# Kernel optimization log

Measured on AMD Instinct MI355X. Metric: run time of the kernel, lower is better.

## Reference

```python
import jax, jax.numpy as jnp
import numpy as np

S = 1024      # seq_len (capped by module's precomputed rows/cols tables)
B = 8         # batch
E = 512       # embed_dim
PD = 192      # pos_dim
H = 8         # num_heads
QHD = 32      # query_head_dim (== key_head_dim)
PHD = 4       # pos_head_dim
IN_DIM = (2 * QHD + PHD) * H  # 544


def setup_inputs() -> dict:
    key = jax.random.key(0)
    k0, k1, k2, k3 = jax.random.split(key, 4)
    x = jax.random.normal(k0, (S, B, E), jnp.float32)
    pos_emb = jax.random.normal(k1, (B, 2 * S - 1, PD), jnp.float32)
    # ScaledLinear(embed_dim, in_proj_dim, initial_scale=query_head_dim**-0.25)
    W_in = jax.random.normal(k2, (E, IN_DIM), jnp.float32) * (QHD ** -0.25) / np.sqrt(E).astype(np.float32)
    b_in = jnp.zeros((IN_DIM,), jnp.float32)
    # ScaledLinear(pos_dim, num_heads*pos_head_dim, bias=False, initial_scale=0.05)
    W_pos = jax.random.normal(k3, (PD, H * PHD), jnp.float32) * (0.05 / np.sqrt(PD).astype(np.float32))
    return {"x": x, "pos_emb": pos_emb, "W_in": W_in, "b_in": b_in, "W_pos": W_pos}


def reference(x, pos_emb, W_in, b_in, W_pos):
    s, b, _ = x.shape
    h, qhd, phd = H, QHD, PHD
    qdim = h * qhd

    proj = x @ W_in + b_in                      # [S, B, 544]
    q = proj[..., :qdim].reshape(s, b, h, qhd)          # [S,B,H,Dq]
    k = proj[..., qdim:2 * qdim].reshape(s, b, h, qhd)  # [S,B,H,Dq]
    p = proj[..., 2 * qdim:].reshape(s, b, h, phd)      # [S,B,H,Dp]

    # attn_scores[h,b,i,j] = q_i . k_j
    attn_scores = jnp.einsum('sbhd,tbhd->hbst', q, k)   # [H,B,S,S]

    # positional projection: [B, 2S-1, H, Dp]
    pe = (pos_emb @ W_pos).reshape(b, 2 * s - 1, h, phd)
    pos_scores = jnp.einsum('sbhd,bnhd->hbsn', p, pe)   # [H,B,S,2S-1]

    # relative skew: index[i,j] = (S-1-i) + j  (matches rows[-S:]+cols gather)
    idx = (s - 1) - jnp.arange(s)[:, None] + jnp.arange(s)[None, :]  # [S,S]
    idx_b = jnp.broadcast_to(idx[None, None], (h, b, s, s))
    rel = jnp.take_along_axis(pos_scores, idx_b, axis=-1)            # [H,B,S,S]

    return jax.nn.softmax(attn_scores + rel, axis=-1)
```

## Files before the change

### kernel.cpp

```cpp
#include <hip/hip_runtime.h>
#include <hip/hip_fp16.h>

#define S_LEN 1024
#define BATCH 8
#define EMB 512
#define POSD 192
#define NH 8
#define QHD 32
#define PHD 4
#define IN_DIM 544
#define QDIM 256
#define NPOS 2047

typedef _Float16 half8 __attribute__((ext_vector_type(8)));
typedef _Float16 half4_t __attribute__((ext_vector_type(4)));
typedef _Float16 half2_t __attribute__((ext_vector_type(2)));
typedef float f32x4 __attribute__((ext_vector_type(4)));

static __device__ __forceinline__ float fdot2(half2_t a, half2_t b, float c) {
#if __has_builtin(__builtin_amdgcn_fdot2)
  return __builtin_amdgcn_fdot2(a, b, c, false);
#else
  return c + (float)a[0] * (float)b[0] + (float)a[1] * (float)b[1];
#endif
}

__global__ __launch_bounds__(256) void wconv_kernel(const float* __restrict__ W_in,
                                                    const float* __restrict__ W_pos,
                                                    _Float16* __restrict__ Wt,
                                                    _Float16* __restrict__ WtP) {
  const int blk = blockIdx.x;
  const int tid = threadIdx.x;
  if (blk < 72) {
    __shared__ float T[64][65];
    const int bx = blk % 9;
    const int by = blk / 9;
    const int n0 = bx * 64, e0 = by * 64;
    const int r = tid >> 4, c4 = (tid & 15) * 4;
    if (n0 + c4 < IN_DIM) {
      #pragma unroll
      for (int rr = 0; rr < 64; rr += 16) {
        f32x4 v = *(const f32x4*)(W_in + (size_t)(e0 + r + rr) * IN_DIM + n0 + c4);
        T[r + rr][c4] = v[0]; T[r + rr][c4 + 1] = v[1];
        T[r + rr][c4 + 2] = v[2]; T[r + rr][c4 + 3] = v[3];
      }
    }
    __syncthreads();
    const int nl = tid >> 2, ec = (tid & 3) * 16;
    const int n = n0 + nl;
    if (n < IN_DIM) {
      half8 h0, h1;
      #pragma unroll
      for (int j = 0; j < 8; ++j) {
        h0[j] = (_Float16)T[ec + j][nl];
        h1[j] = (_Float16)T[ec + 8 + j][nl];
      }
      *(half8*)(Wt + (size_t)n * EMB + e0 + ec) = h0;
      *(half8*)(Wt + (size_t)n * EMB + e0 + ec + 8) = h1;
    }
  } else {
    for (int i = tid; i < 32 * POSD; i += 256) {
      int c = i / POSD, k = i % POSD;
      WtP[i] = (_Float16)W_pos[(size_t)k * 32 + c];
    }
  }
}

__global__ __launch_bounds__(256) void pe_kernel(const float* __restrict__ pos_emb,
                                                 const _Float16* __restrict__ WtP,
                                                 _Float16* __restrict__ pe16) {
  __shared__ __align__(16) _Float16 As[64][200];
  const int b = blockIdx.y, chunk = blockIdx.x;
  const int n0 = chunk * 64;
  const int tid = threadIdx.x;
  const int row = tid >> 2, sc = tid & 3;
  const bool rowok = (n0 + row) < NPOS;
  const float* src = pos_emb + ((size_t)b * NPOS + n0 + row) * POSD + sc * 48;
  #pragma unroll
  for (int j = 0; j < 6; ++j) {
    f32x4 v0 = {}, v1 = {};
    if (rowok) { v0 = *(const f32x4*)(src + j * 8); v1 = *(const f32x4*)(src + j * 8 + 4); }
    half8 h;
    #pragma unroll
    for (int t = 0; t < 4; ++t) { h[t] = (_Float16)v0[t]; h[4 + t] = (_Float16)v1[t]; }
    *(half8*)&As[row][sc * 48 + j * 8] = h;
  }
  __syncthreads();
  const int w = tid >> 6, l = tid & 63, g = l >> 4, lg = l & 15;
  f32x4 acc0 = {}, acc1 = {};
  #pragma unroll
  for (int kk = 0; kk < POSD; kk += 32) {
    half8 aF = *(const half8*)&As[w * 16 + lg][kk + g * 8];
    half8 b0 = *(const half8*)(WtP + (size_t)lg * POSD + kk + g * 8);
    half8 b1 = *(const half8*)(WtP + (size_t)(16 + lg) * POSD + kk + g * 8);
    acc0 = __builtin_amdgcn_mfma_f32_16x16x32_f16(aF, b0, acc0, 0, 0, 0);
    acc1 = __builtin_amdgcn_mfma_f32_16x16x32_f16(aF, b1, acc1, 0, 0, 0);
  }
  f32x4 accs[2] = {acc0, acc1};
  #pragma unroll
  for (int t = 0; t < 2; ++t) {
    int c = t * 16 + lg, h = c >> 2, d = c & 3;
    _Float16* dst = pe16 + ((size_t)(b * NH + h) * NPOS) * PHD + d;
    #pragma unroll
    for (int r = 0; r < 4; ++r) {
      int n = n0 + w * 16 + 4 * g + r;
      if (n < NPOS) dst[(size_t)n * PHD] = (_Float16)accs[t][r];
    }
  }
}

__global__ __launch_bounds__(256) void proj_kernel(const float* __restrict__ x,
                                                   const _Float16* __restrict__ Wt,
                                                   const float* __restrict__ bias,
                                                   _Float16* __restrict__ q16,
                                                   _Float16* __restrict__ k16,
                                                   _Float16* __restrict__ p16) {
  __shared__ __align__(16) _Float16 As[64][40];
  __shared__ __align__(16) _Float16 Bs[64][40];
  const int m0 = blockIdx.x * 64;
  const int n0 = blockIdx.y * 64;
  const int tid = threadIdx.x;
  const int w = tid >> 6, l = tid & 63, g = l >> 4, lg = l & 15;
  const int wm = w >> 1, wn = w & 1;
  const int srow = tid >> 2, sc = tid & 3;

  f32x4 acc[2][2] = {};

  for (int k0 = 0; k0 < EMB; k0 += 32) {
    const float* asrc = x + (size_t)(m0 + srow) * EMB + k0 + sc * 8;
    f32x4 a0 = *(const f32x4*)asrc;
    f32x4 a1 = *(const f32x4*)(asrc + 4);
    half8 ah;
    #pragma unroll
    for (int j = 0; j < 4; ++j) { ah[j] = (_Float16)a0[j]; ah[4 + j] = (_Float16)a1[j]; }
    int nrow = n0 + srow;
    half8 bh8 = {};
    if (nrow < IN_DIM) bh8 = *(const half8*)(Wt + (size_t)nrow * EMB + k0 + sc * 8);
    *(half8*)&As[srow][sc * 8] = ah;
    *(half8*)&Bs[srow][sc * 8] = bh8;
    __syncthreads();
    half8 aF0 = *(const half8*)&As[wm * 32 + lg][g * 8];
    half8 aF1 = *(const half8*)&As[wm * 32 + 16 + lg][g * 8];
    half8 bF0 = *(const half8*)&Bs[wn * 32 + lg][g * 8];
    half8 bF1 = *(const half8*)&Bs[wn * 32 + 16 + lg][g * 8];
    acc[0][0] = __builtin_amdgcn_mfma_f32_16x16x32_f16(aF0, bF0, acc[0][0], 0, 0, 0);
    acc[0][1] = __builtin_amdgcn_mfma_f32_16x16x32_f16(aF0, bF1, acc[0][1], 0, 0, 0);
    acc[1][0] = __builtin_amdgcn_mfma_f32_16x16x32_f16(aF1, bF0, acc[1][0], 0, 0, 0);
    acc[1][1] = __builtin_amdgcn_mfma_f32_16x16x32_f16(aF1, bF1, acc[1][1], 0, 0, 0);
    __syncthreads();
  }

  #pragma unroll
  for (int sm = 0; sm < 2; ++sm)
    #pragma unroll
    for (int sn = 0; sn < 2; ++sn)
      #pragma unroll
      for (int r = 0; r < 4; ++r) {
        int m = m0 + wm * 32 + sm * 16 + 4 * g + r;
        int n = n0 + wn * 32 + sn * 16 + lg;
        if (n < IN_DIM) {
          float v = acc[sm][sn][r] + bias[n];
          _Float16 hv = (_Float16)v;
          int s = m >> 3, b = m & 7;
          if (n < QDIM) {
            int h = n >> 5, d = n & 31;
            q16[(((size_t)(b * NH + h)) * S_LEN + s) * QHD + d] = hv;
          } else if (n < 2 * QDIM) {
            int n2 = n - QDIM;
            int h = n2 >> 5, d = n2 & 31;
            k16[(((size_t)(b * NH + h)) * S_LEN + s) * QHD + d] = hv;
          } else {
            int n2 = n - 2 * QDIM;
            int h = n2 >> 2, d = n2 & 3;
            p16[(((size_t)(b * NH + h)) * S_LEN + s) * PHD + d] = hv;
          }
        }
      }
}

__global__ __launch_bounds__(256, 4) void attn_kernel(const _Float16* __restrict__ q16,
                                                      const _Float16* __restrict__ k16,
                                                      const _Float16* __restrict__ p16,
                                                      const _Float16* __restrict__ pe16,
                                                      float* __restrict__ out) {
  __shared__ __align__(16) _Float16 peLDS[1040 * 4];
  __shared__ float wred[4][16];
  __shared__ __align__(16) float sbuf[4][16][68];
  const int bid = blockIdx.x;
  const int swz = (bid & 7) * 512 + (bid >> 3);
  const int bh = swz >> 6;
  const int rblk = swz & 63;
  const int b = bh >> 3, h = bh & 7;
  const int i0 = rblk * 16;
  const int tid = threadIdx.x;
  const int w = tid >> 6, l = tid & 63, g = l >> 4, lg = l & 15;
  const int nlo = S_LEN - 16 - i0;

  for (int it = tid; it < 1039; it += 256) {
    *(uint2*)&peLDS[it * 4] =
        *(const uint2*)&pe16[((size_t)bh * NPOS + nlo + it) * 4];
  }

  const _Float16* qbase = q16 + ((size_t)bh * S_LEN + i0) * QHD;
  half8 qF = *(const half8*)(qbase + lg * QHD + g * 8);

  const _Float16* pbase = p16 + ((size_t)bh * S_LEN + i0 + lg) * PHD;
  half2_t pq0 = *(const half2_t*)(pbase);
  half2_t pq1 = *(const half2_t*)(pbase + 2);

  __syncthreads();

  const _Float16* kbase = k16 + (size_t)bh * S_LEN * QHD;
  const int jw = w * 256;
  f32x4 zero = {};
  float s = 0.f;
  half4_t probs[16];

  #pragma unroll
  for (int ct = 0; ct < 16; ++ct) {
    int j = jw + ct * 16 + lg;
    half8 kF = *(const half8*)(kbase + (size_t)j * QHD + g * 8);
    f32x4 a = __builtin_amdgcn_mfma_f32_16x16x32_f16(kF, qF, zero, 0, 0, 0);
    int nl0 = 15 - lg + jw + ct * 16 + 4 * g;
    half4_t ph;
    #pragma unroll
    for (int r = 0; r < 4; ++r) {
      half4_t pv4 = *(const half4_t*)&peLDS[(nl0 + r) * 4];
      half2_t lo = {pv4[0], pv4[1]};
      half2_t hi = {pv4[2], pv4[3]};
      float sc = fdot2(pq1, hi, fdot2(pq0, lo, a[r]));
      float e = __expf(sc - 6.0f);
      s += e;
      ph[r] = (_Float16)e;
    }
    probs[ct] = ph;
  }

  s += __shfl_xor(s, 16);
  s += __shfl_xor(s, 32);
  if (g == 0) wred[w][lg] = s;
  __syncthreads();
  s = (wred[0][lg] + wred[1][lg]) + (wred[2][lg] + wred[3][lg]);
  const float inv = 1.0f / s;

  const size_t orow0 = ((size_t)(h * BATCH + b) * S_LEN + i0) * S_LEN;
  #pragma unroll
  for (int chunk = 0; chunk < 4; ++chunk) {
    #pragma unroll
    for (int cc = 0; cc < 4; ++cc) {
      half4_t ph = probs[chunk * 4 + cc];
      f32x4 v;
      #pragma unroll
      for (int r = 0; r < 4; ++r) v[r] = (float)ph[r] * inv;
      *(f32x4*)&sbuf[w][lg][cc * 16 + 4 * g] = v;
    }
    asm volatile("s_waitcnt lgkmcnt(0)" ::: "memory");
    __builtin_amdgcn_sched_barrier(0);
    #pragma unroll
    for (int k2 = 0; k2 < 4; ++k2) {
      int rr = k2 * 4 + g;
      f32x4 v = *(const f32x4*)&sbuf[w][rr][lg * 4];
      __builtin_nontemporal_store(
          v, (f32x4*)(out + orow0 + (size_t)rr * S_LEN + jw + chunk * 64 + lg * 4));
    }
    asm volatile("s_waitcnt lgkmcnt(0)" ::: "memory");
    __builtin_amdgcn_sched_barrier(0);
  }
}

extern "C" void kernel_launch(void* const* d_in, const int* in_sizes, int n_in,
                              void* d_out, int out_size, void* d_ws, size_t ws_size,
                              hipStream_t stream) {
  const float* x = (const float*)d_in[0];
  const float* pos_emb = (const float*)d_in[1];
  const float* W_in = (const float*)d_in[2];
  const float* b_in = (const float*)d_in[3];
  const float* W_pos = (const float*)d_in[4];
  float* out = (float*)d_out;

  char* ws = (char*)d_ws;
  _Float16* Wt = (_Float16*)(ws);
  _Float16* q16 = (_Float16*)(ws + 557056);
  _Float16* k16 = (_Float16*)(ws + 557056 + 4194304);
  _Float16* p16 = (_Float16*)(ws + 557056 + 2 * 4194304);
  _Float16* pe16 = (_Float16*)(ws + 557056 + 2 * 4194304 + 524288);
  _Float16* WtP = p16;

  wconv_kernel<<<dim3(73), dim3(256), 0, stream>>>(W_in, W_pos, Wt, WtP);
  pe_kernel<<<dim3(32, BATCH), dim3(256), 0, stream>>>(pos_emb, WtP, pe16);
  proj_kernel<<<dim3(128, 9), dim3(256), 0, stream>>>(x, Wt, b_in, q16, k16, p16);
  attn_kernel<<<dim3(4096), dim3(256), 0, stream>>>(q16, k16, p16, pe16, out);
}
```

Before: 88.15 us.

## Restructure projection GEMM to stage full x rows once and stream weights

The projection kernel now loads a 32-row slab of x across the whole K dimension into LDS once, converting it to fp16, and covers all 544 output columns in a single block. Each of 8 waves owns 4-5 column tiles and reads weight fragments directly from global memory. This removes the per-K-step double __syncthreads and the 9x re-reading of x across column blocks. In exchange, weights are read without LDS staging, per-block LDS grows, and register use rises with 10 accumulators per wave.

```diff
diff --git a/kernel.cpp b/kernel.cpp
--- a/kernel.cpp
+++ b/kernel.cpp
@@ -109,57 +109,60 @@
   }
 }
 
-__global__ __launch_bounds__(256) void proj_kernel(const float* __restrict__ x,
+__global__ __launch_bounds__(512) void proj_kernel(const float* __restrict__ x,
                                                    const _Float16* __restrict__ Wt,
                                                    const float* __restrict__ bias,
                                                    _Float16* __restrict__ q16,
                                                    _Float16* __restrict__ k16,
                                                    _Float16* __restrict__ p16) {
-  __shared__ __align__(16) _Float16 As[64][40];
-  __shared__ __align__(16) _Float16 Bs[64][40];
-  const int m0 = blockIdx.x * 64;
-  const int n0 = blockIdx.y * 64;
-  const int tid = threadIdx.x;
+  __shared__ __align__(16) _Float16 As[32][520];
+  const int m0 = blockIdx.x * 32;
+  const int tid = threadIdx.x;
+  {
+    const int row = tid >> 4, c0 = (tid & 15) * 32;
+    const float* src = x + (size_t)(m0 + row) * EMB + c0;
+    #pragma unroll
+    for (int jj = 0; jj < 4; ++jj) {
+      f32x4 v0 = *(const f32x4*)(src + jj * 8);
+      f32x4 v1 = *(const f32x4*)(src + jj * 8 + 4);
+      half8 h;
+      #pragma unroll
+      for (int t = 0; t < 4; ++t) { h[t] = (_Float16)v0[t]; h[4 + t] = (_Float16)v1[t]; }
+      *(half8*)&As[row][c0 + jj * 8] = h;
+    }
+  }
+  __syncthreads();
+
   const int w = tid >> 6, l = tid & 63, g = l >> 4, lg = l & 15;
-  const int wm = w >> 1, wn = w & 1;
-  const int srow = tid >> 2, sc = tid & 3;
-
-  f32x4 acc[2][2] = {};
-
-  for (int k0 = 0; k0 < EMB; k0 += 32) {
-    const float* asrc = x + (size_t)(m0 + srow) * EMB + k0 + sc * 8;
-    f32x4 a0 = *(const f32x4*)asrc;
-    f32x4 a1 = *(const f32x4*)(asrc + 4);
-    half8 ah;
-    #pragma unroll
-    for (int j = 0; j < 4; ++j) { ah[j] = (_Float16)a0[j]; ah[4 + j] = (_Float16)a1[j]; }
-    int nrow = n0 + srow;
-    half8 bh8 = {};
-    if (nrow < IN_DIM) bh8 = *(const half8*)(Wt + (size_t)nrow * EMB + k0 + sc * 8);
-    *(half8*)&As[srow][sc * 8] = ah;
-    *(half8*)&Bs[srow][sc * 8] = bh8;
-    __syncthreads();
-    half8 aF0 = *(const half8*)&As[wm * 32 + lg][g * 8];
-    half8 aF1 = *(const half8*)&As[wm * 32 + 16 + lg][g * 8];
-    half8 bF0 = *(const half8*)&Bs[wn * 32 + lg][g * 8];
-    half8 bF1 = *(const half8*)&Bs[wn * 32 + 16 + lg][g * 8];
-    acc[0][0] = __builtin_amdgcn_mfma_f32_16x16x32_f16(aF0, bF0, acc[0][0], 0, 0, 0);
-    acc[0][1] = __builtin_amdgcn_mfma_f32_16x16x32_f16(aF0, bF1, acc[0][1], 0, 0, 0);
-    acc[1][0] = __builtin_amdgcn_mfma_f32_16x16x32_f16(aF1, bF0, acc[1][0], 0, 0, 0);
-    acc[1][1] = __builtin_amdgcn_mfma_f32_16x16x32_f16(aF1, bF1, acc[1][1], 0, 0, 0);
-    __syncthreads();
-  }
-
-  #pragma unroll
-  for (int sm = 0; sm < 2; ++sm)
-    #pragma unroll
-    for (int sn = 0; sn < 2; ++sn)
-      #pragma unroll
-      for (int r = 0; r < 4; ++r) {
-        int m = m0 + wm * 32 + sm * 16 + 4 * g + r;
-        int n = n0 + wn * 32 + sn * 16 + lg;
-        if (n < IN_DIM) {
-          float v = acc[sm][sn][r] + bias[n];
+  const int NT = (w < 2) ? 5 : 4;
+  f32x4 acc[2][5] = {};
+
+  for (int kk = 0; kk < EMB; kk += 32) {
+    half8 a0 = *(const half8*)&As[lg][kk + g * 8];
+    half8 a1 = *(const half8*)&As[16 + lg][kk + g * 8];
+    #pragma unroll
+    for (int tt = 0; tt < 5; ++tt) {
+      if (tt < NT) {
+        int t = w + 8 * tt;
+        half8 bF = *(const half8*)(Wt + (size_t)(t * 16 + lg) * EMB + kk + g * 8);
+        acc[0][tt] = __builtin_amdgcn_mfma_f32_16x16x32_f16(a0, bF, acc[0][tt], 0, 0, 0);
+        acc[1][tt] = __builtin_amdgcn_mfma_f32_16x16x32_f16(a1, bF, acc[1][tt], 0, 0, 0);
+      }
+    }
+  }
+
+  #pragma unroll
+  for (int tt = 0; tt < 5; ++tt) {
+    if (tt < NT) {
+      int t = w + 8 * tt;
+      int n = t * 16 + lg;
+      float bv = bias[n];
+      #pragma unroll
+      for (int fm = 0; fm < 2; ++fm) {
+        #pragma unroll
+        for (int r = 0; r < 4; ++r) {
+          int m = m0 + fm * 16 + 4 * g + r;
+          float v = acc[fm][tt][r] + bv;
           _Float16 hv = (_Float16)v;
           int s = m >> 3, b = m & 7;
           if (n < QDIM) {
@@ -176,6 +179,8 @@
           }
         }
       }
+    }
+  }
 }
 
 __global__ __launch_bounds__(256, 4) void attn_kernel(const _Float16* __restrict__ q16,
@@ -288,6 +293,6 @@
 
   wconv_kernel<<<dim3(73), dim3(256), 0, stream>>>(W_in, W_pos, Wt, WtP);
   pe_kernel<<<dim3(32, BATCH), dim3(256), 0, stream>>>(pos_emb, WtP, pe16);
-  proj_kernel<<<dim3(128, 9), dim3(256), 0, stream>>>(x, Wt, b_in, q16, k16, p16);
+  proj_kernel<<<dim3(256), dim3(512), 0, stream>>>(x, Wt, b_in, q16, k16, p16);
   attn_kernel<<<dim3(4096), dim3(256), 0, stream>>>(q16, k16, p16, pe16, out);
 }
```

New measurement: 94.43 us. 1.07x slower.

## Merge weight conversion and positional projection into one prep kernel; XCD-aware proj tiling

Applied to the files above, without the earlier changes.

Fuses the W_in transpose/convert kernel and the positional-embedding projection kernel into a single launch. Each pe block now converts W_pos into LDS itself instead of reading a global fp16 copy, which removes one launch and the dependency between the two. The proj kernel grid is flattened to 1D and remapped so that consecutive blocks on the same XCD share M tiles, aiming for better L2 reuse of x. The cost is redundant W_pos conversion in every pe block and higher LDS use per block.

```diff
diff --git a/kernel.cpp b/kernel.cpp
--- a/kernel.cpp
+++ b/kernel.cpp
@@ -25,14 +25,16 @@
 #endif
 }
 
-__global__ __launch_bounds__(256) void wconv_kernel(const float* __restrict__ W_in,
-                                                    const float* __restrict__ W_pos,
-                                                    _Float16* __restrict__ Wt,
-                                                    _Float16* __restrict__ WtP) {
+__global__ __launch_bounds__(256) void prep_kernel(const float* __restrict__ W_in,
+                                                   const float* __restrict__ W_pos,
+                                                   const float* __restrict__ pos_emb,
+                                                   _Float16* __restrict__ Wt,
+                                                   _Float16* __restrict__ pe16) {
+  __shared__ __align__(16) char smem[38400];
   const int blk = blockIdx.x;
   const int tid = threadIdx.x;
   if (blk < 72) {
-    __shared__ float T[64][65];
+    float (*T)[65] = reinterpret_cast<float(*)[65]>(smem);
     const int bx = blk % 9;
     const int by = blk / 9;
     const int n0 = bx * 64, e0 = by * 64;
@@ -59,52 +61,52 @@
       *(half8*)(Wt + (size_t)n * EMB + e0 + ec + 8) = h1;
     }
   } else {
-    for (int i = tid; i < 32 * POSD; i += 256) {
-      int c = i / POSD, k = i % POSD;
-      WtP[i] = (_Float16)W_pos[(size_t)k * 32 + c];
-    }
-  }
-}
-
-__global__ __launch_bounds__(256) void pe_kernel(const float* __restrict__ pos_emb,
-                                                 const _Float16* __restrict__ WtP,
-                                                 _Float16* __restrict__ pe16) {
-  __shared__ __align__(16) _Float16 As[64][200];
-  const int b = blockIdx.y, chunk = blockIdx.x;
-  const int n0 = chunk * 64;
-  const int tid = threadIdx.x;
-  const int row = tid >> 2, sc = tid & 3;
-  const bool rowok = (n0 + row) < NPOS;
-  const float* src = pos_emb + ((size_t)b * NPOS + n0 + row) * POSD + sc * 48;
-  #pragma unroll
-  for (int j = 0; j < 6; ++j) {
-    f32x4 v0 = {}, v1 = {};
-    if (rowok) { v0 = *(const f32x4*)(src + j * 8); v1 = *(const f32x4*)(src + j * 8 + 4); }
-    half8 h;
-    #pragma unroll
-    for (int t = 0; t < 4; ++t) { h[t] = (_Float16)v0[t]; h[4 + t] = (_Float16)v1[t]; }
-    *(half8*)&As[row][sc * 48 + j * 8] = h;
-  }
-  __syncthreads();
-  const int w = tid >> 6, l = tid & 63, g = l >> 4, lg = l & 15;
-  f32x4 acc0 = {}, acc1 = {};
-  #pragma unroll
-  for (int kk = 0; kk < POSD; kk += 32) {
-    half8 aF = *(const half8*)&As[w * 16 + lg][kk + g * 8];
-    half8 b0 = *(const half8*)(WtP + (size_t)lg * POSD + kk + g * 8);
-    half8 b1 = *(const half8*)(WtP + (size_t)(16 + lg) * POSD + kk + g * 8);
-    acc0 = __builtin_amdgcn_mfma_f32_16x16x32_f16(aF, b0, acc0, 0, 0, 0);
-    acc1 = __builtin_amdgcn_mfma_f32_16x16x32_f16(aF, b1, acc1, 0, 0, 0);
-  }
-  f32x4 accs[2] = {acc0, acc1};
-  #pragma unroll
-  for (int t = 0; t < 2; ++t) {
-    int c = t * 16 + lg, h = c >> 2, d = c & 3;
-    _Float16* dst = pe16 + ((size_t)(b * NH + h) * NPOS) * PHD + d;
-    #pragma unroll
-    for (int r = 0; r < 4; ++r) {
-      int n = n0 + w * 16 + 4 * g + r;
-      if (n < NPOS) dst[(size_t)n * PHD] = (_Float16)accs[t][r];
+    _Float16 (*As)[200] = reinterpret_cast<_Float16(*)[200]>(smem);
+    _Float16 (*Wl)[200] = reinterpret_cast<_Float16(*)[200]>(smem + 25600);
+    const int id = blk - 72;
+    const int chunk = id & 31, b = id >> 5;
+    const int n0 = chunk * 64;
+    #pragma unroll
+    for (int p = 0; p < 6; ++p) {
+      int f = (p * 256 + tid) * 4;
+      f32x4 v = *(const f32x4*)(W_pos + f);
+      int k = f >> 5, c = f & 31;
+      #pragma unroll
+      for (int t = 0; t < 4; ++t) Wl[c + t][k] = (_Float16)v[t];
+    }
+    const int row = tid >> 2, sc = tid & 3;
+    const bool rowok = (n0 + row) < NPOS;
+    const float* src = pos_emb + ((size_t)b * NPOS + n0 + row) * POSD + sc * 48;
+    #pragma unroll
+    for (int j = 0; j < 6; ++j) {
+      f32x4 v0 = {}, v1 = {};
+      if (rowok) { v0 = *(const f32x4*)(src + j * 8); v1 = *(const f32x4*)(src + j * 8 + 4); }
+      half8 h;
+      #pragma unroll
+      for (int t = 0; t < 4; ++t) { h[t] = (_Float16)v0[t]; h[4 + t] = (_Float16)v1[t]; }
+      *(half8*)&As[row][sc * 48 + j * 8] = h;
+    }
+    __syncthreads();
+    const int w = tid >> 6, l = tid & 63, g = l >> 4, lg = l & 15;
+    f32x4 acc0 = {}, acc1 = {};
+    #pragma unroll
+    for (int kk = 0; kk < POSD; kk += 32) {
+      half8 aF = *(const half8*)&As[w * 16 + lg][kk + g * 8];
+      half8 b0 = *(const half8*)&Wl[lg][kk + g * 8];
+      half8 b1 = *(const half8*)&Wl[16 + lg][kk + g * 8];
+      acc0 = __builtin_amdgcn_mfma_f32_16x16x32_f16(aF, b0, acc0, 0, 0, 0);
+      acc1 = __builtin_amdgcn_mfma_f32_16x16x32_f16(aF, b1, acc1, 0, 0, 0);
+    }
+    f32x4 accs[2] = {acc0, acc1};
+    #pragma unroll
+    for (int t = 0; t < 2; ++t) {
+      int c = t * 16 + lg, h = c >> 2, d = c & 3;
+      _Float16* dst = pe16 + ((size_t)(b * NH + h) * NPOS) * PHD + d;
+      #pragma unroll
+      for (int r2 = 0; r2 < 4; ++r2) {
+        int n = n0 + w * 16 + 4 * g + r2;
+        if (n < NPOS) dst[(size_t)n * PHD] = (_Float16)accs[t][r2];
+      }
     }
   }
 }
@@ -117,8 +119,12 @@
                                                    _Float16* __restrict__ p16) {
   __shared__ __align__(16) _Float16 As[64][40];
   __shared__ __align__(16) _Float16 Bs[64][40];
-  const int m0 = blockIdx.x * 64;
-  const int n0 = blockIdx.y * 64;
+  const int bid = blockIdx.x;
+  const int xcd = bid & 7, idx = bid >> 3;
+  const int mt = xcd * 16 + (idx & 15);
+  const int nt = idx >> 4;
+  const int m0 = mt * 64;
+  const int n0 = nt * 64;
   const int tid = threadIdx.x;
   const int w = tid >> 6, l = tid & 63, g = l >> 4, lg = l & 15;
   const int wm = w >> 1, wn = w & 1;
@@ -284,10 +290,8 @@
   _Float16* k16 = (_Float16*)(ws + 557056 + 4194304);
   _Float16* p16 = (_Float16*)(ws + 557056 + 2 * 4194304);
   _Float16* pe16 = (_Float16*)(ws + 557056 + 2 * 4194304 + 524288);
-  _Float16* WtP = p16;
-
-  wconv_kernel<<<dim3(73), dim3(256), 0, stream>>>(W_in, W_pos, Wt, WtP);
-  pe_kernel<<<dim3(32, BATCH), dim3(256), 0, stream>>>(pos_emb, WtP, pe16);
-  proj_kernel<<<dim3(128, 9), dim3(256), 0, stream>>>(x, Wt, b_in, q16, k16, p16);
+
+  prep_kernel<<<dim3(328), dim3(256), 0, stream>>>(W_in, W_pos, pos_emb, Wt, pe16);
+  proj_kernel<<<dim3(1152), dim3(256), 0, stream>>>(x, Wt, b_in, q16, k16, p16);
   attn_kernel<<<dim3(4096), dim3(256), 0, stream>>>(q16, k16, p16, pe16, out);
 }
```

Measured after the change: 82.39 us. -6.5%, faster.
